# Performance work log

Hardware: AMD Instinct MI355X
Metric: run time of the kernel (lower is better)

Reference implementation:

```python
import jax, jax.numpy as jnp
import numpy as np

HID = 128
MAX_NODES = 100000
MAX_EDGES = 300000
EVT_LEN = 4096
NUM_NODE = 20000
NUM_EDGE = 320000
# EVENT_TYPE_ID_MAP: pad=0 start=1 end=2 node-add=3 node-delete=4 edge-add=5 edge-delete=6
NODE_ADD, NODE_DEL = 3, 4


def time_encode(t, time_w, time_b):
    # TimeEncoder: cos(Linear(1 -> hidden)(t))
    return jnp.cos(t[..., None] * time_w + time_b)


def gru_cell(x, h, w_ih, w_hh, b_ih, b_hh):
    gi = x @ w_ih.T + b_ih
    gh = h @ w_hh.T + b_hh
    i_r, i_z, i_n = jnp.split(gi, 3, axis=-1)
    h_r, h_z, h_n = jnp.split(gh, 3, axis=-1)
    r = jax.nn.sigmoid(i_r + h_r)
    z = jax.nn.sigmoid(i_z + h_z)
    n = jnp.tanh(i_n + r * h_n)
    return (1.0 - z) * n + z * h


def setup_inputs() -> dict:
    key = jax.random.key(0)
    ks = jax.random.split(key, 32)
    H = HID
    s = 0.05
    inp = {}
    inp["event_type_ids"] = jax.random.randint(ks[0], (EVT_LEN,), 0, 7)
    inp["src_ids"] = jax.random.randint(ks[1], (EVT_LEN,), 0, MAX_NODES)
    inp["src_mask"] = (jax.random.uniform(ks[2], (EVT_LEN,)) > 0.3).astype(jnp.float32)
    inp["dst_ids"] = jax.random.randint(ks[3], (EVT_LEN,), 0, MAX_NODES)
    inp["dst_mask"] = (jax.random.uniform(ks[4], (EVT_LEN,)) > 0.3).astype(jnp.float32)
    inp["event_edge_ids"] = jax.random.randint(ks[5], (EVT_LEN,), 0, MAX_EDGES)
    inp["event_embeddings"] = jax.random.normal(ks[6], (EVT_LEN, H), dtype=jnp.float32)
    inp["event_mask"] = (jax.random.uniform(ks[7], (EVT_LEN,)) > 0.2).astype(jnp.float32)
    inp["event_timestamps"] = jax.random.uniform(ks[8], (EVT_LEN,)) * 100.0
    inp["node_ids"] = jax.random.randint(ks[9], (NUM_NODE,), 0, MAX_NODES)
    inp["edge_ids"] = jax.random.randint(ks[10], (NUM_EDGE,), 0, MAX_EDGES)
    inp["edge_index"] = jax.random.randint(ks[11], (2, NUM_EDGE), 0, NUM_NODE)
    inp["time"] = 100
    # persistent-buffer state
    inp["memory"] = jax.random.normal(ks[12], (MAX_NODES, H), dtype=jnp.float32) * s
    inp["last_update"] = jax.random.uniform(ks[13], (MAX_EDGES,)) * 50.0
    inp["node_features"] = jax.random.normal(ks[14], (MAX_NODES, H), dtype=jnp.float32) * s
    inp["edge_features"] = jax.random.normal(ks[15], (MAX_EDGES, H), dtype=jnp.float32) * s
    # TimeEncoder params (Linear(1, H))
    inp["time_w"] = jax.random.normal(ks[16], (H,), dtype=jnp.float32) * s
    inp["time_b"] = jax.random.normal(ks[17], (H,), dtype=jnp.float32) * s
    # GRUCell(5H -> H)
    inp["gru_w_ih"] = jax.random.normal(ks[18], (3 * H, 5 * H), dtype=jnp.float32) * s
    inp["gru_w_hh"] = jax.random.normal(ks[19], (3 * H, H), dtype=jnp.float32) * s
    inp["gru_b_ih"] = jax.random.normal(ks[20], (3 * H,), dtype=jnp.float32) * s
    inp["gru_b_hh"] = jax.random.normal(ks[21], (3 * H,), dtype=jnp.float32) * s
    # TransformerConv(H, H, heads=1, edge_dim=2H)
    inp["wq"] = jax.random.normal(ks[22], (H, H), dtype=jnp.float32) * s
    inp["bq"] = jax.random.normal(ks[23], (H,), dtype=jnp.float32) * s
    inp["wk"] = jax.random.normal(ks[24], (H, H), dtype=jnp.float32) * s
    inp["bk"] = jax.random.normal(ks[25], (H,), dtype=jnp.float32) * s
    inp["wv"] = jax.random.normal(ks[26], (H, H), dtype=jnp.float32) * s
    inp["bv"] = jax.random.normal(ks[27], (H,), dtype=jnp.float32) * s
    inp["we"] = jax.random.normal(ks[28], (H, 2 * H), dtype=jnp.float32) * s  # lin_edge, no bias
    inp["wskip"] = jax.random.normal(ks[29], (H, H), dtype=jnp.float32) * s
    inp["bskip"] = jax.random.normal(ks[30], (H,), dtype=jnp.float32) * s
    return inp


def reference(event_type_ids, src_ids, src_mask, dst_ids, dst_mask, event_edge_ids,
              event_embeddings, event_mask, event_timestamps, node_ids, edge_ids,
              edge_index, time, memory, last_update, node_features, edge_features,
              time_w, time_b, gru_w_ih, gru_w_hh, gru_b_ih, gru_b_hh,
              wq, bq, wk, bk, wv, bv, we, wskip, bskip):
    H = HID
    # ---- message() ----
    L = event_type_ids.shape[0]
    type_embs = jnp.broadcast_to(event_type_ids[:, None].astype(memory.dtype), (L, H))
    src_embs = memory[src_ids] * src_mask[:, None]
    dst_embs = memory[dst_ids] * dst_mask[:, None]
    edge_last = last_update[event_edge_ids]
    rel_ts = event_timestamps - edge_last * dst_mask
    is_node_ev = ((event_type_ids == NODE_ADD) | (event_type_ids == NODE_DEL)).astype(event_timestamps.dtype)
    ts_emb = time_encode(event_timestamps * is_node_ev + rel_ts * dst_mask, time_w, time_b) * event_mask[:, None]
    src_msgs = jnp.concatenate([type_embs, src_embs, dst_embs, ts_emb, event_embeddings], axis=1) * event_mask[:, None]
    dst_msgs = jnp.concatenate([type_embs, dst_embs, src_embs, ts_emb, event_embeddings], axis=1) * dst_mask[:, None]
    # ---- agg_message(): scatter-mean over node ids ----
    def agg(msgs, ids):
        s = jax.ops.segment_sum(msgs, ids, num_segments=MAX_NODES)
        c = jax.ops.segment_sum(jnp.ones((msgs.shape[0],), msgs.dtype), ids, num_segments=MAX_NODES)
        return s / jnp.maximum(c, 1.0)[:, None]
    agg_src = agg(src_msgs, src_ids)
    agg_dst = agg(dst_msgs, dst_ids)
    # ---- GRU memory update on unique ids ----
    # torch: memory[cat(uniq_src, uniq_dst)] = rnn(...); reads use pre-update memory,
    # dst writes come after src writes so they override on overlap. Duplicate ids in
    # src_ids carry identical per-id values, so scatter-set is equivalent to unique().
    new_src = gru_cell(agg_src[src_ids], memory[src_ids], gru_w_ih, gru_w_hh, gru_b_ih, gru_b_hh)
    new_dst = gru_cell(agg_dst[dst_ids], memory[dst_ids], gru_w_ih, gru_w_hh, gru_b_ih, gru_b_hh)
    memory = memory.at[src_ids].set(new_src)
    memory = memory.at[dst_ids].set(new_dst)
    # ---- edge attributes ----
    rel_t = time - last_update[edge_ids]
    rel_t_embs = time_encode(rel_t, time_w, time_b)
    edge_attr = jnp.concatenate([rel_t_embs, edge_features[edge_ids]], axis=-1)  # (E, 2H)
    # ---- TransformerConv (heads=1, concat, root_weight) ----
    x = node_features[node_ids] + memory[node_ids]  # (N, H)
    src, dst = edge_index[0], edge_index[1]
    q = x @ wq.T + bq
    k = x @ wk.T + bk
    v = x @ wv.T + bv
    e = edge_attr @ we.T  # lin_edge (no bias)
    alpha = jnp.sum(q[dst] * (k[src] + e), axis=-1) / jnp.sqrt(jnp.asarray(H, x.dtype))
    amax = jax.ops.segment_max(alpha, dst, num_segments=x.shape[0])
    ex = jnp.exp(alpha - amax[dst])
    denom = jax.ops.segment_sum(ex, dst, num_segments=x.shape[0])
    p = ex / jnp.maximum(denom[dst], 1e-16)
    out = jax.ops.segment_sum(p[:, None] * (v[src] + e), dst, num_segments=x.shape[0])
    return out + x @ wskip.T + bskip
```

## Files before the change

kernel.cpp:

```cpp
#include <hip/hip_runtime.h>
#include <math.h>

#define HID   128
#define MAXN  100000
#define MAXE  300000
#define EVT   4096
#define NNODE 20000
#define NEDGE 320000

typedef unsigned short u16;
typedef __attribute__((ext_vector_type(8))) short bf16x8;
typedef __attribute__((ext_vector_type(4))) float f32x4;

#define OFF_WIHB      0u
#define OFF_WHHB      491520u
#define OFF_WEB       589824u
#define OFF_WALLB     655360u
#define OFF_BALL      851968u
#define BASE2         855040u
#define OFF_REP_SRC   (BASE2 + 0u)
#define OFF_REP_DST   (BASE2 + 400128u)
#define OFF_CNT_SRC   (BASE2 + 800256u)
#define OFF_CNT_DST   (BASE2 + 1200384u)
#define OFF_SUM_SRC   (BASE2 + 1600512u)
#define OFF_SUM_DST   (BASE2 + 12086272u)
#define OFF_XGB       (BASE2 + 22572032u)
#define OFF_HG        (BASE2 + 33057792u)
#define OFF_HGB       (BASE2 + 37252096u)
#define OFF_GI        (BASE2 + 39349248u)
#define OFF_GH        (BASE2 + 51932160u)
#define OFF_NEWMEM    (BASE2 + 64515072u)
#define OFF_XB        (BASE2 + 0u)
#define OFF_QKVSE     (BASE2 + 5120000u)
#define OFF_KVB       (BASE2 + 66560000u)
#define OFF_DEG       (BASE2 + 76800000u)
#define OFF_OFFS      (BASE2 + 76880128u)
#define OFF_CURSOR    (BASE2 + 76960256u)
#define OFF_BSUM      (BASE2 + 77040384u)
#define OFF_SORTED    (BASE2 + 77041664u)
#define OFF_SACCB     (BASE2 + 78321664u)

__device__ __forceinline__ float sigmoidf_(float x) { return 1.f / (1.f + __expf(-x)); }
__device__ __forceinline__ u16 f2b(float f) {
    unsigned u = __float_as_uint(f);
    unsigned r = (u + 0x7fffu + ((u >> 16) & 1u)) >> 16;
    return (u16)r;
}
__device__ __forceinline__ float b2f(unsigned h) { return __uint_as_float(h << 16); }

__global__ void k_cvt(const float* __restrict__ s, u16* __restrict__ d, int n) {
    int i = blockIdx.x * blockDim.x + threadIdx.x;
    if (i < n) d[i] = f2b(s[i]);
}

__global__ void k_tables(const int* __restrict__ src_ids, const int* __restrict__ dst_ids,
                         unsigned* rep_src, unsigned* rep_dst, int* cnt_src, int* cnt_dst) {
    int i = blockIdx.x * blockDim.x + threadIdx.x;
    if (i >= EVT) return;
    int s = src_ids[i], d = dst_ids[i];
    atomicMin(&rep_src[s], (unsigned)i);
    atomicAdd(&cnt_src[s], 1);
    atomicMin(&rep_dst[d], (unsigned)i);
    atomicAdd(&cnt_dst[d], 1);
}

__global__ void k_message(const int* __restrict__ et_ids, const int* __restrict__ src_ids,
                          const float* __restrict__ src_mask, const int* __restrict__ dst_ids,
                          const float* __restrict__ dst_mask, const int* __restrict__ ev_eids,
                          const float* __restrict__ ev_emb, const float* __restrict__ ev_mask,
                          const float* __restrict__ ev_ts, const float* __restrict__ memory,
                          const float* __restrict__ last_update, const float* __restrict__ time_w,
                          const float* __restrict__ time_b, const unsigned* __restrict__ rep_src,
                          const unsigned* __restrict__ rep_dst, const int* __restrict__ cnt_src,
                          const int* __restrict__ cnt_dst, float* sum_src, float* sum_dst) {
    int i = blockIdx.x;
    int c = threadIdx.x;
    int et = et_ids[i];
    float sm = src_mask[i], dm = dst_mask[i], em = ev_mask[i], ts = ev_ts[i];
    int sid = src_ids[i], did = dst_ids[i], eid = ev_eids[i];
    float isnode = (et == 3 || et == 4) ? 1.f : 0.f;
    float rel = ts - last_update[eid] * dm;
    float tval = ts * isnode + rel * dm;
    float tse = __cosf(tval * time_w[c] + time_b[c]) * em;
    float typ = (float)et;
    float sv = memory[(size_t)sid * HID + c] * sm;
    float dv = memory[(size_t)did * HID + c] * dm;
    float ev = ev_emb[(size_t)i * HID + c];
    float* ps = sum_src + (size_t)rep_src[sid] * 640;
    if (cnt_src[sid] == 1) {
        ps[c] = typ * em; ps[128 + c] = sv * em; ps[256 + c] = dv * em;
        ps[384 + c] = tse * em; ps[512 + c] = ev * em;
    } else {
        atomicAdd(ps + c, typ * em);
        atomicAdd(ps + 128 + c, sv * em);
        atomicAdd(ps + 256 + c, dv * em);
        atomicAdd(ps + 384 + c, tse * em);
        atomicAdd(ps + 512 + c, ev * em);
    }
    float* pd = sum_dst + (size_t)rep_dst[did] * 640;
    if (cnt_dst[did] == 1) {
        pd[c] = typ * dm; pd[128 + c] = dv * dm; pd[256 + c] = sv * dm;
        pd[384 + c] = tse * dm; pd[512 + c] = ev * dm;
    } else {
        atomicAdd(pd + c, typ * dm);
        atomicAdd(pd + 128 + c, dv * dm);
        atomicAdd(pd + 256 + c, sv * dm);
        atomicAdd(pd + 384 + c, tse * dm);
        atomicAdd(pd + 512 + c, ev * dm);
    }
}

__global__ void k_build_xg(const int* __restrict__ src_ids, const int* __restrict__ dst_ids,
                           const unsigned* __restrict__ rep_src, const unsigned* __restrict__ rep_dst,
                           const int* __restrict__ cnt_src, const int* __restrict__ cnt_dst,
                           const float* __restrict__ sum_src, const float* __restrict__ sum_dst,
                           u16* __restrict__ Xgb) {
    int r = blockIdx.x;
    int c = blockIdx.y * 128 + threadIdx.x;
    float v;
    if (r < EVT) {
        int id = src_ids[r];
        int cnt = cnt_src[id]; if (cnt < 1) cnt = 1;
        v = sum_src[(size_t)rep_src[id] * 640 + c] / (float)cnt;
    } else {
        int id = dst_ids[r - EVT];
        int cnt = cnt_dst[id]; if (cnt < 1) cnt = 1;
        v = sum_dst[(size_t)rep_dst[id] * 640 + c] / (float)cnt;
    }
    Xgb[(size_t)r * 640 + c] = f2b(v);
}

__global__ void k_build_hg(const int* __restrict__ src_ids, const int* __restrict__ dst_ids,
                           const float* __restrict__ memory, float* __restrict__ Hg,
                           u16* __restrict__ Hgb) {
    int r = blockIdx.x, c = threadIdx.x;
    int id = (r < EVT) ? src_ids[r] : dst_ids[r - EVT];
    float v = memory[(size_t)id * HID + c];
    Hg[(size_t)r * HID + c] = v;
    Hgb[(size_t)r * HID + c] = f2b(v);
}

__global__ __launch_bounds__(256) void k_gemm_mfma(const u16* __restrict__ A,
                                                   const u16* __restrict__ W,
                                                   const float* __restrict__ bias,
                                                   float* __restrict__ C,
                                                   u16* __restrict__ KVb,
                                                   int M, int N, int K, int acc) {
    __shared__ u16 Als[128 * 40];
    __shared__ u16 Wls[128 * 40];
    int tid = threadIdx.x;
    int bm = blockIdx.x * 128, bn = blockIdx.y * 128;
    int wave = tid >> 6, lane = tid & 63;
    int wm = (wave & 1) * 64, wn = (wave >> 1) * 64;
    int l15 = lane & 15, quad = lane >> 4;
    f32x4 accf[4][4] = {};
    for (int k0 = 0; k0 < K; k0 += 32) {
#pragma unroll
        for (int h = 0; h < 2; ++h) {
            int ch = tid + h * 256;
            int row = ch >> 2, kc = (ch & 3) * 8;
            int gr = bm + row;
            float4 av = make_float4(0.f, 0.f, 0.f, 0.f);
            if (gr < M) av = *(const float4*)(A + (size_t)gr * K + k0 + kc);
            *(float4*)&Als[row * 40 + kc] = av;
            int wr = bn + row;
            float4 wv_ = *(const float4*)(W + (size_t)wr * K + k0 + kc);
            *(float4*)&Wls[row * 40 + kc] = wv_;
        }
        __syncthreads();
        bf16x8 af[4], bfr[4];
#pragma unroll
        for (int r = 0; r < 4; ++r)
            af[r] = *(const bf16x8*)&Als[(wm + r * 16 + l15) * 40 + quad * 8];
#pragma unroll
        for (int c2 = 0; c2 < 4; ++c2)
            bfr[c2] = *(const bf16x8*)&Wls[(wn + c2 * 16 + l15) * 40 + quad * 8];
#pragma unroll
        for (int r = 0; r < 4; ++r)
#pragma unroll
            for (int c2 = 0; c2 < 4; ++c2)
                accf[r][c2] = __builtin_amdgcn_mfma_f32_16x16x32_bf16(af[r], bfr[c2], accf[r][c2], 0, 0, 0);
        __syncthreads();
    }
#pragma unroll
    for (int r = 0; r < 4; ++r) {
#pragma unroll
        for (int c2 = 0; c2 < 4; ++c2) {
            int ncol = bn + wn + c2 * 16 + l15;
            float bv = bias ? bias[ncol] : 0.f;
#pragma unroll
            for (int reg = 0; reg < 4; ++reg) {
                int mrow = bm + wm + r * 16 + quad * 4 + reg;
                if (mrow >= M) continue;
                float v = accf[r][c2][reg] + bv;
                if (acc) v += C[(size_t)mrow * N + ncol];
                C[(size_t)mrow * N + ncol] = v;
                if (KVb && ncol >= 128 && ncol < 384)
                    KVb[(size_t)mrow * 256 + (ncol - 128)] = f2b(v);
            }
        }
    }
}

__global__ void k_gru(const float* __restrict__ Gi, const float* __restrict__ Gh,
                      const float* __restrict__ Hg, float* __restrict__ newmem) {
    int r = blockIdx.x, c = threadIdx.x;
    const float* gi = Gi + (size_t)r * 384;
    const float* gh = Gh + (size_t)r * 384;
    float rg = sigmoidf_(gi[c] + gh[c]);
    float z  = sigmoidf_(gi[128 + c] + gh[128 + c]);
    float n  = tanhf(gi[256 + c] + rg * gh[256 + c]);
    float h  = Hg[(size_t)r * HID + c];
    newmem[(size_t)r * HID + c] = (1.f - z) * n + z * h;
}

__global__ void k_scatter(float* __restrict__ memory, const int* __restrict__ ids,
                          const float* __restrict__ newmem) {
    int i = blockIdx.x, c = threadIdx.x;
    memory[(size_t)ids[i] * HID + c] = newmem[(size_t)i * HID + c];
}

__global__ void k_wall(const float* __restrict__ wq, const float* __restrict__ wk_,
                       const float* __restrict__ wv, const float* __restrict__ wskip,
                       const float* __restrict__ we, const float* __restrict__ bq,
                       const float* __restrict__ bk, const float* __restrict__ bv,
                       const float* __restrict__ bskip, u16* __restrict__ Wallb,
                       float* __restrict__ ball) {
    int row = blockIdx.x;
    int k = threadIdx.x;
    float v;
    if (row < 128)      v = wq[row * 128 + k];
    else if (row < 256) v = wk_[(row - 128) * 128 + k];
    else if (row < 384) v = wv[(row - 256) * 128 + k];
    else if (row < 512) v = wskip[(row - 384) * 128 + k];
    else {
        int j = row - 512;
        float a = 0.f;
        for (int t = 0; t < 128; t++) a += wq[t * 128 + k] * we[t * 256 + j];
        v = a;
    }
    Wallb[row * 128 + k] = f2b(v);
    if (k == 0) {
        float b;
        if (row < 128)      b = bq[row];
        else if (row < 256) b = bk[row - 128];
        else if (row < 384) b = bv[row - 256];
        else if (row < 512) b = bskip[row - 384];
        else { int j = row - 512; float a = 0.f; for (int t = 0; t < 128; t++) a += bq[t] * we[t * 256 + j]; b = a; }
        ball[row] = b;
    }
}

__global__ void k_x(const int* __restrict__ node_ids, const float* __restrict__ nf,
                    const float* __restrict__ memory, u16* __restrict__ Xb) {
    int p = blockIdx.x, c = threadIdx.x;
    int nid = node_ids[p];
    Xb[(size_t)p * HID + c] = f2b(nf[(size_t)nid * HID + c] + memory[(size_t)nid * HID + c]);
}

__global__ void k_deg(const int* __restrict__ eidx, int* __restrict__ deg) {
    int j = blockIdx.x * blockDim.x + threadIdx.x;
    if (j >= NEDGE) return;
    atomicAdd(&deg[eidx[NEDGE + j]], 1);
}

__global__ __launch_bounds__(256) void k_scan1(const int* __restrict__ deg,
                                               int* __restrict__ offs, int* __restrict__ bsum) {
    __shared__ int wsum[4];
    int i = blockIdx.x * 256 + threadIdx.x;
    int v = (i < NNODE) ? deg[i] : 0;
    int lane = threadIdx.x & 63, w = threadIdx.x >> 6;
    int x = v;
#pragma unroll
    for (int d = 1; d < 64; d <<= 1) { int y = __shfl_up(x, d, 64); if (lane >= d) x += y; }
    if (lane == 63) wsum[w] = x;
    __syncthreads();
    int add = 0;
    for (int k = 0; k < w; ++k) add += wsum[k];
    int incl = x + add;
    if (i < NNODE) offs[i] = incl - v;
    if (threadIdx.x == 255) bsum[blockIdx.x] = incl;
}

__global__ __launch_bounds__(128) void k_scan2(int* __restrict__ bsum, int nb) {
    __shared__ int w0s;
    int t = threadIdx.x;
    int v = (t < nb) ? bsum[t] : 0;
    int lane = t & 63, w = t >> 6;
    int x = v;
#pragma unroll
    for (int d = 1; d < 64; d <<= 1) { int y = __shfl_up(x, d, 64); if (lane >= d) x += y; }
    if (t == 63) w0s = x;
    __syncthreads();
    if (w == 1) x += w0s;
    if (t < nb) bsum[t] = x - v;
}

__global__ __launch_bounds__(256) void k_scan3(int* __restrict__ offs, const int* __restrict__ bsum,
                                               int* __restrict__ cursor) {
    int i = blockIdx.x * 256 + threadIdx.x;
    if (i < NNODE) { int o = offs[i] + bsum[blockIdx.x]; offs[i] = o; cursor[i] = o; }
    if (i == 0) offs[NNODE] = NEDGE;
}

__global__ void k_sortscat(const int* __restrict__ eidx, int* __restrict__ cursor,
                           int* __restrict__ sorted) {
    int j = blockIdx.x * blockDim.x + threadIdx.x;
    if (j >= NEDGE) return;
    int d = eidx[NEDGE + j];
    int pos = atomicAdd(&cursor[d], 1);
    sorted[pos] = j;
}

__global__ __launch_bounds__(256) void k_node(const float* __restrict__ QK,
        const u16* __restrict__ KVb, const int* __restrict__ offs,
        const int* __restrict__ sorted, const int* __restrict__ eidx,
        const int* __restrict__ edge_ids, const float* __restrict__ last_update,
        const float* __restrict__ time_w, const float* __restrict__ time_b,
        const float* __restrict__ ef, const int* __restrict__ tptr,
        float* __restrict__ out, u16* __restrict__ saccb) {
    int wave = threadIdx.x >> 6, lane = threadIdx.x & 63;
    int n = blockIdx.x * 4 + wave;
    int c = 2 * lane;
    const float* base = QK + (size_t)n * 768;
    float2 qd   = *(const float2*)(base + c);
    float2 skip = *(const float2*)(base + 384 + c);
    float2 qet  = *(const float2*)(base + 512 + c);
    float2 qef  = *(const float2*)(base + 640 + c);
    float2 tw   = *(const float2*)(time_w + c);
    float2 tb   = *(const float2*)(time_b + c);
    float tf = (float)(*tptr);
    int start = offs[n], end = offs[n + 1];
    int deg = end - start;
    if (deg == 0) {
        *(float2*)(out + (size_t)n * HID + c) = skip;
        *(unsigned*)(saccb + (size_t)n * 256 + c) = 0u;
        *(unsigned*)(saccb + (size_t)n * 256 + 128 + c) = 0u;
        return;
    }
    float m = -1e30f, l_ = 0.f;
    float va0 = 0.f, va1 = 0.f, s00 = 0.f, s01 = 0.f, s10 = 0.f, s11 = 0.f;
    for (int cb = start; cb < end; cb += 64) {
        int cnt = end - cb; if (cnt > 64) cnt = 64;
        int s_l = 0, eid_l = 0; float rt_l = 0.f;
        if (lane < cnt) {
            int j = sorted[cb + lane];
            s_l = eidx[j];
            eid_l = edge_ids[j];
            rt_l = tf - last_update[eid_l];
        }
        for (int e0 = 0; e0 < cnt; e0 += 4) {
            float pv[4], cv0[4], cv1[4], vx[4], vy[4], ex[4], ey[4];
#pragma unroll
            for (int i = 0; i < 4; ++i) {
                int idx = e0 + i;
                int sel = (idx < cnt) ? idx : e0;
                int s   = __shfl(s_l, sel, 64);
                int eid = __shfl(eid_l, sel, 64);
                float rt = __shfl(rt_l, sel, 64);
                unsigned kvp = *(const unsigned*)(KVb + (size_t)s * 256 + c);
                unsigned vvp = *(const unsigned*)(KVb + (size_t)s * 256 + 128 + c);
                float2 ev = *(const float2*)(ef + (size_t)eid * HID + c);
                float k0f = b2f(kvp & 0xffffu), k1f = b2f(kvp >> 16);
                vx[i] = b2f(vvp & 0xffffu); vy[i] = b2f(vvp >> 16);
                cv0[i] = __cosf(rt * tw.x + tb.x);
                cv1[i] = __cosf(rt * tw.y + tb.y);
                ex[i] = ev.x; ey[i] = ev.y;
                pv[i] = qd.x * k0f + qd.y * k1f + qet.x * cv0[i] + qet.y * cv1[i]
                      + qef.x * ev.x + qef.y * ev.y;
            }
#pragma unroll
            for (int msk = 32; msk > 0; msk >>= 1) {
#pragma unroll
                for (int i = 0; i < 4; ++i) pv[i] += __shfl_xor(pv[i], msk, 64);
            }
            float al[4];
#pragma unroll
            for (int i = 0; i < 4; ++i)
                al[i] = (e0 + i < cnt) ? pv[i] * 0.08838834764831845f : -1e30f;
            float gm = fmaxf(fmaxf(al[0], al[1]), fmaxf(al[2], al[3]));
            if (gm > m) {
                float fac = __expf(m - gm);
                l_ *= fac; va0 *= fac; va1 *= fac;
                s00 *= fac; s01 *= fac; s10 *= fac; s11 *= fac;
                m = gm;
            }
#pragma unroll
            for (int i = 0; i < 4; ++i) {
                float w = __expf(al[i] - m);
                l_ += w;
                va0 += w * vx[i]; va1 += w * vy[i];
                s00 += w * cv0[i]; s01 += w * cv1[i];
                s10 += w * ex[i]; s11 += w * ey[i];
            }
        }
    }
    float inv = 1.f / fmaxf(l_, 1e-16f);
    float2 o; o.x = va0 * inv + skip.x; o.y = va1 * inv + skip.y;
    *(float2*)(out + (size_t)n * HID + c) = o;
    unsigned p0 = (unsigned)f2b(s00 * inv) | ((unsigned)f2b(s01 * inv) << 16);
    unsigned p1 = (unsigned)f2b(s10 * inv) | ((unsigned)f2b(s11 * inv) << 16);
    *(unsigned*)(saccb + (size_t)n * 256 + c) = p0;
    *(unsigned*)(saccb + (size_t)n * 256 + 128 + c) = p1;
}

extern "C" void kernel_launch(void* const* d_in, const int* in_sizes, int n_in,
                              void* d_out, int out_size, void* d_ws, size_t ws_size,
                              hipStream_t stream) {
    const int*   et_ids        = (const int*)d_in[0];
    const int*   src_ids       = (const int*)d_in[1];
    const float* src_mask      = (const float*)d_in[2];
    const int*   dst_ids       = (const int*)d_in[3];
    const float* dst_mask      = (const float*)d_in[4];
    const int*   ev_eids       = (const int*)d_in[5];
    const float* ev_emb        = (const float*)d_in[6];
    const float* ev_mask       = (const float*)d_in[7];
    const float* ev_ts         = (const float*)d_in[8];
    const int*   node_ids      = (const int*)d_in[9];
    const int*   edge_ids      = (const int*)d_in[10];
    const int*   edge_index    = (const int*)d_in[11];
    const int*   tptr          = (const int*)d_in[12];
    float*       memory        = (float*)d_in[13];
    const float* last_update   = (const float*)d_in[14];
    const float* node_features = (const float*)d_in[15];
    const float* edge_features = (const float*)d_in[16];
    const float* time_w        = (const float*)d_in[17];
    const float* time_b        = (const float*)d_in[18];
    const float* w_ih          = (const float*)d_in[19];
    const float* w_hh          = (const float*)d_in[20];
    const float* b_ih          = (const float*)d_in[21];
    const float* b_hh          = (const float*)d_in[22];
    const float* wq            = (const float*)d_in[23];
    const float* bq            = (const float*)d_in[24];
    const float* wk            = (const float*)d_in[25];
    const float* bk            = (const float*)d_in[26];
    const float* wv            = (const float*)d_in[27];
    const float* bv            = (const float*)d_in[28];
    const float* we            = (const float*)d_in[29];
    const float* wskip         = (const float*)d_in[30];
    const float* bskip         = (const float*)d_in[31];
    float* out = (float*)d_out;
    char*  wsb = (char*)d_ws;

    u16*   w_ih_b  = (u16*)(wsb + OFF_WIHB);
    u16*   w_hh_b  = (u16*)(wsb + OFF_WHHB);
    u16*   we_b    = (u16*)(wsb + OFF_WEB);
    u16*   Wallb   = (u16*)(wsb + OFF_WALLB);
    float* ball    = (float*)(wsb + OFF_BALL);
    unsigned* rep_src = (unsigned*)(wsb + OFF_REP_SRC);
    unsigned* rep_dst = (unsigned*)(wsb + OFF_REP_DST);
    int*   cnt_src = (int*)(wsb + OFF_CNT_SRC);
    int*   cnt_dst = (int*)(wsb + OFF_CNT_DST);
    float* sum_src = (float*)(wsb + OFF_SUM_SRC);
    float* sum_dst = (float*)(wsb + OFF_SUM_DST);
    u16*   Xgb     = (u16*)(wsb + OFF_XGB);
    float* Hg      = (float*)(wsb + OFF_HG);
    u16*   Hgb     = (u16*)(wsb + OFF_HGB);
    float* Gi      = (float*)(wsb + OFF_GI);
    float* Gh      = (float*)(wsb + OFF_GH);
    float* newmem  = (float*)(wsb + OFF_NEWMEM);
    u16*   Xb      = (u16*)(wsb + OFF_XB);
    float* QKVSE   = (float*)(wsb + OFF_QKVSE);
    u16*   KVb     = (u16*)(wsb + OFF_KVB);
    int*   deg     = (int*)(wsb + OFF_DEG);
    int*   offs    = (int*)(wsb + OFF_OFFS);
    int*   cursor  = (int*)(wsb + OFF_CURSOR);
    int*   bsum    = (int*)(wsb + OFF_BSUM);
    int*   sorted  = (int*)(wsb + OFF_SORTED);
    u16*   saccb   = (u16*)(wsb + OFF_SACCB);

    k_cvt<<<(384 * 640 + 255) / 256, 256, 0, stream>>>(w_ih, w_ih_b, 384 * 640);
    k_cvt<<<(384 * 128 + 255) / 256, 256, 0, stream>>>(w_hh, w_hh_b, 384 * 128);
    k_cvt<<<(128 * 256 + 255) / 256, 256, 0, stream>>>(we, we_b, 128 * 256);
    k_wall<<<768, 128, 0, stream>>>(wq, wk, wv, wskip, we, bq, bk, bv, bskip, Wallb, ball);

    hipMemsetAsync(wsb + OFF_REP_SRC, 0xFF, 800256, stream);
    hipMemsetAsync(wsb + OFF_CNT_SRC, 0, 800256, stream);
    hipMemsetAsync(wsb + OFF_SUM_SRC, 0, 2u * 10485760u, stream);
    k_tables<<<16, 256, 0, stream>>>(src_ids, dst_ids, rep_src, rep_dst, cnt_src, cnt_dst);
    k_message<<<EVT, 128, 0, stream>>>(et_ids, src_ids, src_mask, dst_ids, dst_mask, ev_eids,
                                       ev_emb, ev_mask, ev_ts, memory, last_update, time_w, time_b,
                                       rep_src, rep_dst, cnt_src, cnt_dst, sum_src, sum_dst);
    k_build_xg<<<dim3(2 * EVT, 5), 128, 0, stream>>>(src_ids, dst_ids, rep_src, rep_dst,
                                                     cnt_src, cnt_dst, sum_src, sum_dst, Xgb);
    k_build_hg<<<2 * EVT, 128, 0, stream>>>(src_ids, dst_ids, memory, Hg, Hgb);
    k_gemm_mfma<<<dim3(64, 3), 256, 0, stream>>>(Xgb, w_ih_b, b_ih, Gi, nullptr, 2 * EVT, 384, 640, 0);
    k_gemm_mfma<<<dim3(64, 3), 256, 0, stream>>>(Hgb, w_hh_b, b_hh, Gh, nullptr, 2 * EVT, 384, 128, 0);
    k_gru<<<2 * EVT, 128, 0, stream>>>(Gi, Gh, Hg, newmem);
    k_scatter<<<EVT, 128, 0, stream>>>(memory, src_ids, newmem);
    k_scatter<<<EVT, 128, 0, stream>>>(memory, dst_ids, newmem + (size_t)EVT * HID);

    k_x<<<NNODE, 128, 0, stream>>>(node_ids, node_features, memory, Xb);
    k_gemm_mfma<<<dim3(157, 6), 256, 0, stream>>>(Xb, Wallb, ball, QKVSE, KVb, NNODE, 768, 128, 0);
    hipMemsetAsync(wsb + OFF_DEG, 0, 80128, stream);
    k_deg<<<1250, 256, 0, stream>>>(edge_index, deg);
    k_scan1<<<79, 256, 0, stream>>>(deg, offs, bsum);
    k_scan2<<<1, 128, 0, stream>>>(bsum, 79);
    k_scan3<<<79, 256, 0, stream>>>(offs, bsum, cursor);
    k_sortscat<<<1250, 256, 0, stream>>>(edge_index, cursor, sorted);
    k_node<<<NNODE / 4, 256, 0, stream>>>(QKVSE, KVb, offs, sorted, edge_index, edge_ids,
                                          last_update, time_w, time_b, edge_features, tptr,
                                          out, saccb);
    k_gemm_mfma<<<dim3(157, 1), 256, 0, stream>>>(saccb, we_b, nullptr, out, nullptr, NNODE, 128, 256, 1);
}
```

Baseline: 559.4 us.

## Fuse prep kernels, drop big memset, merge GRU+scatter, compact QKV output, single-block scan

Merges the weight-conversion kernels into one prep launch. Replaces the 20MB memset of the message sums with targeted zeroing of only the duplicate-representative rows. Folds the Hg gather into the message kernel and fuses the GRU update with the memory scatter. The QKV GEMM now writes a compact Q/skip/edge-q buffer instead of the full 768-wide fp32 output, the three-kernel scan becomes one 1024-thread block, and the node attention loop is unrolled to 8 edges per step. The single-block scan serialises that step, and the wider unroll raises register pressure.

```diff
diff --git a/kernel.cpp b/kernel.cpp
--- a/kernel.cpp
+++ b/kernel.cpp
@@ -29,16 +29,14 @@
 #define OFF_HGB       (BASE2 + 37252096u)
 #define OFF_GI        (BASE2 + 39349248u)
 #define OFF_GH        (BASE2 + 51932160u)
-#define OFF_NEWMEM    (BASE2 + 64515072u)
 #define OFF_XB        (BASE2 + 0u)
-#define OFF_QKVSE     (BASE2 + 5120000u)
-#define OFF_KVB       (BASE2 + 66560000u)
-#define OFF_DEG       (BASE2 + 76800000u)
-#define OFF_OFFS      (BASE2 + 76880128u)
-#define OFF_CURSOR    (BASE2 + 76960256u)
-#define OFF_BSUM      (BASE2 + 77040384u)
-#define OFF_SORTED    (BASE2 + 77041664u)
-#define OFF_SACCB     (BASE2 + 78321664u)
+#define OFF_QS        (BASE2 + 5120000u)
+#define OFF_KVB       (BASE2 + 46080000u)
+#define OFF_DEG       (BASE2 + 56320000u)
+#define OFF_OFFS      (BASE2 + 56400128u)
+#define OFF_CURSOR    (BASE2 + 56480256u)
+#define OFF_SORTED    (BASE2 + 56560384u)
+#define OFF_SACCB     (BASE2 + 57840384u)
 
 __device__ __forceinline__ float sigmoidf_(float x) { return 1.f / (1.f + __expf(-x)); }
 __device__ __forceinline__ u16 f2b(float f) {
@@ -48,9 +46,41 @@
 }
 __device__ __forceinline__ float b2f(unsigned h) { return __uint_as_float(h << 16); }
 
-__global__ void k_cvt(const float* __restrict__ s, u16* __restrict__ d, int n) {
-    int i = blockIdx.x * blockDim.x + threadIdx.x;
-    if (i < n) d[i] = f2b(s[i]);
+__global__ __launch_bounds__(256) void k_prep(const float* __restrict__ w_ih, u16* __restrict__ w_ih_b,
+                       const float* __restrict__ w_hh, u16* __restrict__ w_hh_b,
+                       const float* __restrict__ we, u16* __restrict__ we_b,
+                       const float* __restrict__ wq, const float* __restrict__ wk_,
+                       const float* __restrict__ wv, const float* __restrict__ wskip,
+                       const float* __restrict__ bq, const float* __restrict__ bk,
+                       const float* __restrict__ bv, const float* __restrict__ bskip,
+                       u16* __restrict__ Wallb, float* __restrict__ ball) {
+    int b = blockIdx.x, t = threadIdx.x;
+    if (b < 960) { int i = b * 256 + t; w_ih_b[i] = f2b(w_ih[i]); return; }
+    if (b < 1152) { int i = (b - 960) * 256 + t; w_hh_b[i] = f2b(w_hh[i]); return; }
+    if (b < 1280) { int i = (b - 1152) * 256 + t; we_b[i] = f2b(we[i]); return; }
+    int idx = (b - 1280) * 256 + t;
+    int row = idx >> 7, k = idx & 127;
+    float v;
+    if (row < 128)      v = wq[row * 128 + k];
+    else if (row < 256) v = wk_[(row - 128) * 128 + k];
+    else if (row < 384) v = wv[(row - 256) * 128 + k];
+    else if (row < 512) v = wskip[(row - 384) * 128 + k];
+    else {
+        int j = row - 512;
+        float a = 0.f;
+        for (int q = 0; q < 128; q++) a += wq[q * 128 + k] * we[q * 256 + j];
+        v = a;
+    }
+    Wallb[row * 128 + k] = f2b(v);
+    if (k == 0) {
+        float bb;
+        if (row < 128)      bb = bq[row];
+        else if (row < 256) bb = bk[row - 128];
+        else if (row < 384) bb = bv[row - 256];
+        else if (row < 512) bb = bskip[row - 384];
+        else { int j = row - 512; float a = 0.f; for (int q = 0; q < 128; q++) a += bq[q] * we[q * 256 + j]; bb = a; }
+        ball[row] = bb;
+    }
 }
 
 __global__ void k_tables(const int* __restrict__ src_ids, const int* __restrict__ dst_ids,
@@ -64,6 +94,24 @@
     atomicAdd(&cnt_dst[d], 1);
 }
 
+__global__ void k_zerodup(const int* __restrict__ src_ids, const int* __restrict__ dst_ids,
+                          const unsigned* __restrict__ rep_src, const unsigned* __restrict__ rep_dst,
+                          const int* __restrict__ cnt_src, const int* __restrict__ cnt_dst,
+                          float* sum_src, float* sum_dst) {
+    int i = blockIdx.x, c = threadIdx.x;
+    int sid = src_ids[i], did = dst_ids[i];
+    if (cnt_src[sid] > 1 && rep_src[sid] == (unsigned)i) {
+        float* p = sum_src + (size_t)i * 640;
+#pragma unroll
+        for (int h = 0; h < 5; ++h) p[h * 128 + c] = 0.f;
+    }
+    if (cnt_dst[did] > 1 && rep_dst[did] == (unsigned)i) {
+        float* p = sum_dst + (size_t)i * 640;
+#pragma unroll
+        for (int h = 0; h < 5; ++h) p[h * 128 + c] = 0.f;
+    }
+}
+
 __global__ void k_message(const int* __restrict__ et_ids, const int* __restrict__ src_ids,
                           const float* __restrict__ src_mask, const int* __restrict__ dst_ids,
                           const float* __restrict__ dst_mask, const int* __restrict__ ev_eids,
@@ -72,7 +120,8 @@
                           const float* __restrict__ last_update, const float* __restrict__ time_w,
                           const float* __restrict__ time_b, const unsigned* __restrict__ rep_src,
                           const unsigned* __restrict__ rep_dst, const int* __restrict__ cnt_src,
-                          const int* __restrict__ cnt_dst, float* sum_src, float* sum_dst) {
+                          const int* __restrict__ cnt_dst, float* sum_src, float* sum_dst,
+                          float* __restrict__ Hg, u16* __restrict__ Hgb) {
     int i = blockIdx.x;
     int c = threadIdx.x;
     int et = et_ids[i];
@@ -83,8 +132,13 @@
     float tval = ts * isnode + rel * dm;
     float tse = __cosf(tval * time_w[c] + time_b[c]) * em;
     float typ = (float)et;
-    float sv = memory[(size_t)sid * HID + c] * sm;
-    float dv = memory[(size_t)did * HID + c] * dm;
+    float m_s = memory[(size_t)sid * HID + c];
+    float m_d = memory[(size_t)did * HID + c];
+    Hg[(size_t)i * HID + c] = m_s;
+    Hgb[(size_t)i * HID + c] = f2b(m_s);
+    Hg[(size_t)(EVT + i) * HID + c] = m_d;
+    Hgb[(size_t)(EVT + i) * HID + c] = f2b(m_d);
+    float sv = m_s * sm, dv = m_d * dm;
     float ev = ev_emb[(size_t)i * HID + c];
     float* ps = sum_src + (size_t)rep_src[sid] * 640;
     if (cnt_src[sid] == 1) {
@@ -130,22 +184,12 @@
     Xgb[(size_t)r * 640 + c] = f2b(v);
 }
 
-__global__ void k_build_hg(const int* __restrict__ src_ids, const int* __restrict__ dst_ids,
-                           const float* __restrict__ memory, float* __restrict__ Hg,
-                           u16* __restrict__ Hgb) {
-    int r = blockIdx.x, c = threadIdx.x;
-    int id = (r < EVT) ? src_ids[r] : dst_ids[r - EVT];
-    float v = memory[(size_t)id * HID + c];
-    Hg[(size_t)r * HID + c] = v;
-    Hgb[(size_t)r * HID + c] = f2b(v);
-}
-
 __global__ __launch_bounds__(256) void k_gemm_mfma(const u16* __restrict__ A,
                                                    const u16* __restrict__ W,
                                                    const float* __restrict__ bias,
-                                                   float* __restrict__ C,
+                                                   float* __restrict__ C, int ldc,
                                                    u16* __restrict__ KVb,
-                                                   int M, int N, int K, int acc) {
+                                                   int M, int N, int K, int acc, int special) {
     __shared__ u16 Als[128 * 40];
     __shared__ u16 Wls[128 * 40];
     int tid = threadIdx.x;
@@ -182,73 +226,48 @@
                 accf[r][c2] = __builtin_amdgcn_mfma_f32_16x16x32_bf16(af[r], bfr[c2], accf[r][c2], 0, 0, 0);
         __syncthreads();
     }
+    int y = blockIdx.y;
+    int qsb = -1, kvbase = -1;
+    if (special) {
+        qsb = (y == 0) ? 0 : (y == 3) ? 128 : (y == 4) ? 256 : (y == 5) ? 384 : -1;
+        kvbase = (y == 1) ? 0 : (y == 2) ? 128 : -1;
+    }
 #pragma unroll
     for (int r = 0; r < 4; ++r) {
 #pragma unroll
         for (int c2 = 0; c2 < 4; ++c2) {
-            int ncol = bn + wn + c2 * 16 + l15;
+            int colw = wn + c2 * 16 + l15;
+            int ncol = bn + colw;
             float bv = bias ? bias[ncol] : 0.f;
 #pragma unroll
             for (int reg = 0; reg < 4; ++reg) {
                 int mrow = bm + wm + r * 16 + quad * 4 + reg;
                 if (mrow >= M) continue;
                 float v = accf[r][c2][reg] + bv;
-                if (acc) v += C[(size_t)mrow * N + ncol];
-                C[(size_t)mrow * N + ncol] = v;
-                if (KVb && ncol >= 128 && ncol < 384)
-                    KVb[(size_t)mrow * 256 + (ncol - 128)] = f2b(v);
+                if (special) {
+                    if (qsb >= 0) C[(size_t)mrow * 512 + qsb + colw] = v;
+                    if (kvbase >= 0) KVb[(size_t)mrow * 256 + kvbase + colw] = f2b(v);
+                } else {
+                    if (acc) v += C[(size_t)mrow * ldc + ncol];
+                    C[(size_t)mrow * ldc + ncol] = v;
+                }
             }
         }
     }
 }
 
-__global__ void k_gru(const float* __restrict__ Gi, const float* __restrict__ Gh,
-                      const float* __restrict__ Hg, float* __restrict__ newmem) {
-    int r = blockIdx.x, c = threadIdx.x;
+__global__ void k_gruscat(const float* __restrict__ Gi, const float* __restrict__ Gh,
+                          const float* __restrict__ Hg, const int* __restrict__ ids,
+                          int roff, float* __restrict__ memory) {
+    int b = blockIdx.x, c = threadIdx.x;
+    int r = b + roff;
     const float* gi = Gi + (size_t)r * 384;
     const float* gh = Gh + (size_t)r * 384;
     float rg = sigmoidf_(gi[c] + gh[c]);
     float z  = sigmoidf_(gi[128 + c] + gh[128 + c]);
     float n  = tanhf(gi[256 + c] + rg * gh[256 + c]);
     float h  = Hg[(size_t)r * HID + c];
-    newmem[(size_t)r * HID + c] = (1.f - z) * n + z * h;
-}
-
-__global__ void k_scatter(float* __restrict__ memory, const int* __restrict__ ids,
-                          const float* __restrict__ newmem) {
-    int i = blockIdx.x, c = threadIdx.x;
-    memory[(size_t)ids[i] * HID + c] = newmem[(size_t)i * HID + c];
-}
-
-__global__ void k_wall(const float* __restrict__ wq, const float* __restrict__ wk_,
-                       const float* __restrict__ wv, const float* __restrict__ wskip,
-                       const float* __restrict__ we, const float* __restrict__ bq,
-                       const float* __restrict__ bk, const float* __restrict__ bv,
-                       const float* __restrict__ bskip, u16* __restrict__ Wallb,
-                       float* __restrict__ ball) {
-    int row = blockIdx.x;
-    int k = threadIdx.x;
-    float v;
-    if (row < 128)      v = wq[row * 128 + k];
-    else if (row < 256) v = wk_[(row - 128) * 128 + k];
-    else if (row < 384) v = wv[(row - 256) * 128 + k];
-    else if (row < 512) v = wskip[(row - 384) * 128 + k];
-    else {
-        int j = row - 512;
-        float a = 0.f;
-        for (int t = 0; t < 128; t++) a += wq[t * 128 + k] * we[t * 256 + j];
-        v = a;
-    }
-    Wallb[row * 128 + k] = f2b(v);
-    if (k == 0) {
-        float b;
-        if (row < 128)      b = bq[row];
-        else if (row < 256) b = bk[row - 128];
-        else if (row < 384) b = bv[row - 256];
-        else if (row < 512) b = bskip[row - 384];
-        else { int j = row - 512; float a = 0.f; for (int t = 0; t < 128; t++) a += bq[t] * we[t * 256 + j]; b = a; }
-        ball[row] = b;
-    }
+    memory[(size_t)ids[b] * HID + c] = (1.f - z) * n + z * h;
 }
 
 __global__ void k_x(const int* __restrict__ node_ids, const float* __restrict__ nf,
@@ -264,43 +283,23 @@
     atomicAdd(&deg[eidx[NEDGE + j]], 1);
 }
 
-__global__ __launch_bounds__(256) void k_scan1(const int* __restrict__ deg,
-                                               int* __restrict__ offs, int* __restrict__ bsum) {
-    __shared__ int wsum[4];
-    int i = blockIdx.x * 256 + threadIdx.x;
-    int v = (i < NNODE) ? deg[i] : 0;
-    int lane = threadIdx.x & 63, w = threadIdx.x >> 6;
-    int x = v;
-#pragma unroll
-    for (int d = 1; d < 64; d <<= 1) { int y = __shfl_up(x, d, 64); if (lane >= d) x += y; }
-    if (lane == 63) wsum[w] = x;
-    __syncthreads();
-    int add = 0;
-    for (int k = 0; k < w; ++k) add += wsum[k];
-    int incl = x + add;
-    if (i < NNODE) offs[i] = incl - v;
-    if (threadIdx.x == 255) bsum[blockIdx.x] = incl;
-}
-
-__global__ __launch_bounds__(128) void k_scan2(int* __restrict__ bsum, int nb) {
-    __shared__ int w0s;
+__global__ __launch_bounds__(1024) void k_scan(const int* __restrict__ deg,
+                                               int* __restrict__ offs, int* __restrict__ cursor) {
+    __shared__ int part[1024];
     int t = threadIdx.x;
-    int v = (t < nb) ? bsum[t] : 0;
-    int lane = t & 63, w = t >> 6;
-    int x = v;
-#pragma unroll
-    for (int d = 1; d < 64; d <<= 1) { int y = __shfl_up(x, d, 64); if (lane >= d) x += y; }
-    if (t == 63) w0s = x;
-    __syncthreads();
-    if (w == 1) x += w0s;
-    if (t < nb) bsum[t] = x - v;
-}
-
-__global__ __launch_bounds__(256) void k_scan3(int* __restrict__ offs, const int* __restrict__ bsum,
-                                               int* __restrict__ cursor) {
-    int i = blockIdx.x * 256 + threadIdx.x;
-    if (i < NNODE) { int o = offs[i] + bsum[blockIdx.x]; offs[i] = o; cursor[i] = o; }
-    if (i == 0) offs[NNODE] = NEDGE;
+    int base = t * 20;
+    int loc[20]; int s = 0;
+    for (int i = 0; i < 20; i++) { int idx = base + i; int v = (idx < NNODE) ? deg[idx] : 0; loc[i] = s; s += v; }
+    part[t] = s; __syncthreads();
+    for (int dgap = 1; dgap < 1024; dgap <<= 1) {
+        int v = (t >= dgap) ? part[t - dgap] : 0;
+        __syncthreads();
+        part[t] += v;
+        __syncthreads();
+    }
+    int excl = (t == 0) ? 0 : part[t - 1];
+    for (int i = 0; i < 20; i++) { int idx = base + i; if (idx < NNODE) { int o = excl + loc[i]; offs[idx] = o; cursor[idx] = o; } }
+    if (t == 1023) offs[NNODE] = part[1023];
 }
 
 __global__ void k_sortscat(const int* __restrict__ eidx, int* __restrict__ cursor,
@@ -312,7 +311,7 @@
     sorted[pos] = j;
 }
 
-__global__ __launch_bounds__(256) void k_node(const float* __restrict__ QK,
+__global__ __launch_bounds__(256) void k_node(const float* __restrict__ QS,
         const u16* __restrict__ KVb, const int* __restrict__ offs,
         const int* __restrict__ sorted, const int* __restrict__ eidx,
         const int* __restrict__ edge_ids, const float* __restrict__ last_update,
@@ -322,11 +321,11 @@
     int wave = threadIdx.x >> 6, lane = threadIdx.x & 63;
     int n = blockIdx.x * 4 + wave;
     int c = 2 * lane;
-    const float* base = QK + (size_t)n * 768;
+    const float* base = QS + (size_t)n * 512;
     float2 qd   = *(const float2*)(base + c);
-    float2 skip = *(const float2*)(base + 384 + c);
-    float2 qet  = *(const float2*)(base + 512 + c);
-    float2 qef  = *(const float2*)(base + 640 + c);
+    float2 skip = *(const float2*)(base + 128 + c);
+    float2 qet  = *(const float2*)(base + 256 + c);
+    float2 qef  = *(const float2*)(base + 384 + c);
     float2 tw   = *(const float2*)(time_w + c);
     float2 tb   = *(const float2*)(time_b + c);
     float tf = (float)(*tptr);
@@ -349,10 +348,10 @@
             eid_l = edge_ids[j];
             rt_l = tf - last_update[eid_l];
         }
-        for (int e0 = 0; e0 < cnt; e0 += 4) {
-            float pv[4], cv0[4], cv1[4], vx[4], vy[4], ex[4], ey[4];
-#pragma unroll
-            for (int i = 0; i < 4; ++i) {
+        for (int e0 = 0; e0 < cnt; e0 += 8) {
+            float pv[8], cv0[8], cv1[8], vx[8], vy[8], ex[8], ey[8];
+#pragma unroll
+            for (int i = 0; i < 8; ++i) {
                 int idx = e0 + i;
                 int sel = (idx < cnt) ? idx : e0;
                 int s   = __shfl(s_l, sel, 64);
@@ -372,13 +371,15 @@
 #pragma unroll
             for (int msk = 32; msk > 0; msk >>= 1) {
 #pragma unroll
-                for (int i = 0; i < 4; ++i) pv[i] += __shfl_xor(pv[i], msk, 64);
+                for (int i = 0; i < 8; ++i) pv[i] += __shfl_xor(pv[i], msk, 64);
             }
-            float al[4];
-#pragma unroll
-            for (int i = 0; i < 4; ++i)
+            float al[8];
+#pragma unroll
+            for (int i = 0; i < 8; ++i)
                 al[i] = (e0 + i < cnt) ? pv[i] * 0.08838834764831845f : -1e30f;
-            float gm = fmaxf(fmaxf(al[0], al[1]), fmaxf(al[2], al[3]));
+            float gm = al[0];
+#pragma unroll
+            for (int i = 1; i < 8; ++i) gm = fmaxf(gm, al[i]);
             if (gm > m) {
                 float fac = __expf(m - gm);
                 l_ *= fac; va0 *= fac; va1 *= fac;
@@ -386,7 +387,7 @@
                 m = gm;
             }
 #pragma unroll
-            for (int i = 0; i < 4; ++i) {
+            for (int i = 0; i < 8; ++i) {
                 float w = __expf(al[i] - m);
                 l_ += w;
                 va0 += w * vx[i]; va1 += w * vy[i];
@@ -458,48 +459,42 @@
     u16*   Hgb     = (u16*)(wsb + OFF_HGB);
     float* Gi      = (float*)(wsb + OFF_GI);
     float* Gh      = (float*)(wsb + OFF_GH);
-    float* newmem  = (float*)(wsb + OFF_NEWMEM);
     u16*   Xb      = (u16*)(wsb + OFF_XB);
-    float* QKVSE   = (float*)(wsb + OFF_QKVSE);
+    float* QS      = (float*)(wsb + OFF_QS);
     u16*   KVb     = (u16*)(wsb + OFF_KVB);
     int*   deg     = (int*)(wsb + OFF_DEG);
     int*   offs    = (int*)(wsb + OFF_OFFS);
     int*   cursor  = (int*)(wsb + OFF_CURSOR);
-    int*   bsum    = (int*)(wsb + OFF_BSUM);
     int*   sorted  = (int*)(wsb + OFF_SORTED);
     u16*   saccb   = (u16*)(wsb + OFF_SACCB);
 
-    k_cvt<<<(384 * 640 + 255) / 256, 256, 0, stream>>>(w_ih, w_ih_b, 384 * 640);
-    k_cvt<<<(384 * 128 + 255) / 256, 256, 0, stream>>>(w_hh, w_hh_b, 384 * 128);
-    k_cvt<<<(128 * 256 + 255) / 256, 256, 0, stream>>>(we, we_b, 128 * 256);
-    k_wall<<<768, 128, 0, stream>>>(wq, wk, wv, wskip, we, bq, bk, bv, bskip, Wallb, ball);
+    k_prep<<<1664, 256, 0, stream>>>(w_ih, w_ih_b, w_hh, w_hh_b, we, we_b,
+                                     wq, wk, wv, wskip, bq, bk, bv, bskip, Wallb, ball);
 
     hipMemsetAsync(wsb + OFF_REP_SRC, 0xFF, 800256, stream);
     hipMemsetAsync(wsb + OFF_CNT_SRC, 0, 800256, stream);
-    hipMemsetAsync(wsb + OFF_SUM_SRC, 0, 2u * 10485760u, stream);
     k_tables<<<16, 256, 0, stream>>>(src_ids, dst_ids, rep_src, rep_dst, cnt_src, cnt_dst);
+    k_zerodup<<<EVT, 128, 0, stream>>>(src_ids, dst_ids, rep_src, rep_dst, cnt_src, cnt_dst,
+                                       sum_src, sum_dst);
     k_message<<<EVT, 128, 0, stream>>>(et_ids, src_ids, src_mask, dst_ids, dst_mask, ev_eids,
                                        ev_emb, ev_mask, ev_ts, memory, last_update, time_w, time_b,
-                                       rep_src, rep_dst, cnt_src, cnt_dst, sum_src, sum_dst);
+                                       rep_src, rep_dst, cnt_src, cnt_dst, sum_src, sum_dst,
+                                       Hg, Hgb);
     k_build_xg<<<dim3(2 * EVT, 5), 128, 0, stream>>>(src_ids, dst_ids, rep_src, rep_dst,
                                                      cnt_src, cnt_dst, sum_src, sum_dst, Xgb);
-    k_build_hg<<<2 * EVT, 128, 0, stream>>>(src_ids, dst_ids, memory, Hg, Hgb);
-    k_gemm_mfma<<<dim3(64, 3), 256, 0, stream>>>(Xgb, w_ih_b, b_ih, Gi, nullptr, 2 * EVT, 384, 640, 0);
-    k_gemm_mfma<<<dim3(64, 3), 256, 0, stream>>>(Hgb, w_hh_b, b_hh, Gh, nullptr, 2 * EVT, 384, 128, 0);
-    k_gru<<<2 * EVT, 128, 0, stream>>>(Gi, Gh, Hg, newmem);
-    k_scatter<<<EVT, 128, 0, stream>>>(memory, src_ids, newmem);
-    k_scatter<<<EVT, 128, 0, stream>>>(memory, dst_ids, newmem + (size_t)EVT * HID);
+    k_gemm_mfma<<<dim3(64, 3), 256, 0, stream>>>(Xgb, w_ih_b, b_ih, Gi, 384, nullptr, 2 * EVT, 384, 640, 0, 0);
+    k_gemm_mfma<<<dim3(64, 3), 256, 0, stream>>>(Hgb, w_hh_b, b_hh, Gh, 384, nullptr, 2 * EVT, 384, 128, 0, 0);
+    k_gruscat<<<EVT, 128, 0, stream>>>(Gi, Gh, Hg, src_ids, 0, memory);
+    k_gruscat<<<EVT, 128, 0, stream>>>(Gi, Gh, Hg, dst_ids, EVT, memory);
 
     k_x<<<NNODE, 128, 0, stream>>>(node_ids, node_features, memory, Xb);
-    k_gemm_mfma<<<dim3(157, 6), 256, 0, stream>>>(Xb, Wallb, ball, QKVSE, KVb, NNODE, 768, 128, 0);
+    k_gemm_mfma<<<dim3(157, 6), 256, 0, stream>>>(Xb, Wallb, ball, QS, 512, KVb, NNODE, 768, 128, 0, 1);
     hipMemsetAsync(wsb + OFF_DEG, 0, 80128, stream);
     k_deg<<<1250, 256, 0, stream>>>(edge_index, deg);
-    k_scan1<<<79, 256, 0, stream>>>(deg, offs, bsum);
-    k_scan2<<<1, 128, 0, stream>>>(bsum, 79);
-    k_scan3<<<79, 256, 0, stream>>>(offs, bsum, cursor);
+    k_scan<<<1, 1024, 0, stream>>>(deg, offs, cursor);
     k_sortscat<<<1250, 256, 0, stream>>>(edge_index, cursor, sorted);
-    k_node<<<NNODE / 4, 256, 0, stream>>>(QKVSE, KVb, offs, sorted, edge_index, edge_ids,
+    k_node<<<NNODE / 4, 256, 0, stream>>>(QS, KVb, offs, sorted, edge_index, edge_ids,
                                           last_update, time_w, time_b, edge_features, tptr,
                                           out, saccb);
-    k_gemm_mfma<<<dim3(157, 1), 256, 0, stream>>>(saccb, we_b, nullptr, out, nullptr, NNODE, 128, 256, 1);
-}
+    k_gemm_mfma<<<dim3(157, 1), 256, 0, stream>>>(saccb, we_b, nullptr, out, 128, nullptr, NNODE, 128, 256, 1, 0);
+}
```

New measurement: 564.8 us. Within noise of the previous version (+1.0%).
